# Optimization experiments

Measured on AMD Instinct MI355X. Metric: run time of the kernel, lower is better.

Reference implementation:

```python
import jax, jax.numpy as jnp
import numpy as np

B, OUT_LEN, IN_LEN, H = 8, 1024, 4096, 256


def setup_inputs() -> dict:
    key = jax.random.key(0)
    k1, k2, k3 = jax.random.split(key, 3)
    output = jax.random.normal(k1, (B, OUT_LEN, H), dtype=jnp.float32)
    encoder_outputs = jax.random.normal(k2, (B, IN_LEN, H), dtype=jnp.float32)
    # valid lengths in [1, IN_LEN] so every softmax row has >=1 unmasked entry
    lengths = jax.random.randint(k3, (B,), 1, IN_LEN + 1).astype(jnp.int32)
    return {"output": output, "encoder_outputs": encoder_outputs, "lengths": lengths}


def reference(output, encoder_outputs, lengths):
    # scores: [B, out_len, in_len], unscaled dot-product (as in the original)
    scores = jnp.einsum('boh,bih->boi', output, encoder_outputs)
    # mask[b, j] = j < lengths[b]; masked positions get -inf (additive mask)
    valid = jnp.arange(encoder_outputs.shape[1])[None, :] < lengths[:, None]  # [B, in_len]
    scores = jnp.where(valid[:, None, :], scores, -jnp.inf)
    attn = jax.nn.softmax(scores, axis=-1)  # [B, out_len, in_len]
    context = jnp.einsum('boi,bih->boh', attn, encoder_outputs)  # [B, out_len, H]
    return (context, attn)
```

## Files before the change

### kernel.cpp

```cpp
#include <hip/hip_runtime.h>
#include <hip/hip_bf16.h>
#include <math.h>

#define B_    8
#define OLEN  1024
#define ILEN  4096
#define HDIM  256
#define LDA   40

typedef __attribute__((ext_vector_type(8))) short bf16x8;
typedef __attribute__((ext_vector_type(4))) float f32x4;

__device__ inline unsigned pk_bf16(float x, float y) {
  union { __hip_bfloat162 h; unsigned u; } c;
  c.h = __float22bfloat162_rn(make_float2(x, y));
  return c.u;
}
__device__ inline short f2bf(float x) {
  union { __hip_bfloat16 h; short s; } c;
  c.h = __float2bfloat16(x);
  return c.s;
}

struct HiLo { uint4 hi, lo; };
__device__ inline HiLo split8(const float* __restrict__ p) {
  float4 v0 = *(const float4*)p;
  float4 v1 = *(const float4*)(p + 4);
  float f[8] = {v0.x, v0.y, v0.z, v0.w, v1.x, v1.y, v1.z, v1.w};
  unsigned hu[8]; float lo[8];
#pragma unroll
  for (int i = 0; i < 8; ++i) {
    unsigned u = __float_as_uint(f[i]);
    hu[i] = u & 0xffff0000u;
    lo[i] = f[i] - __uint_as_float(hu[i]);
  }
  HiLo r;
  r.hi = make_uint4((hu[0] >> 16) | hu[1], (hu[2] >> 16) | hu[3],
                    (hu[4] >> 16) | hu[5], (hu[6] >> 16) | hu[7]);
  r.lo = make_uint4(pk_bf16(lo[0], lo[1]), pk_bf16(lo[2], lo[3]),
                    pk_bf16(lo[4], lo[5]), pk_bf16(lo[6], lo[7]));
  return r;
}

__global__ __launch_bounds__(256) void k_etrans(const float* __restrict__ E,
                                                short* __restrict__ ET) {
  const int it = blockIdx.x, ht = blockIdx.y, b = blockIdx.z;
  __shared__ short L[32][36];
  const int t = threadIdx.x;
  {
    const int i = t >> 3, h0 = (t & 7) * 4;
    float4 v = *(const float4*)&E[((size_t)(b * ILEN + it * 32 + i)) * HDIM + ht * 32 + h0];
    L[h0 + 0][i] = f2bf(v.x);
    L[h0 + 1][i] = f2bf(v.y);
    L[h0 + 2][i] = f2bf(v.z);
    L[h0 + 3][i] = f2bf(v.w);
  }
  __syncthreads();
  {
    const int h = t >> 3, i0 = (t & 7) * 4;
    uint2 o = *(const uint2*)&L[h][i0];
    *(uint2*)&ET[((size_t)(b * HDIM + ht * 32 + h)) * ILEN + it * 32 + i0] = o;
  }
}

__global__ __launch_bounds__(256) void k_scores(const float* __restrict__ Q,
                                                const float* __restrict__ E,
                                                float* __restrict__ S) {
  const int b = blockIdx.z, ot = blockIdx.y, it = blockIdx.x;
  const float* Qb = Q + ((size_t)b * OLEN + ot * 64) * HDIM;
  const float* Eb = E + ((size_t)b * ILEN + it * 64) * HDIM;

  __shared__ __align__(16) short Ah[64 * LDA], Al[64 * LDA];
  __shared__ __align__(16) short Bh[64 * LDA], Bl[64 * LDA];

  const int t = threadIdx.x;
  const int w = t >> 6, l = t & 63;
  const int la = l & 15, quad = l >> 4;
  const int sr = t >> 2, sc = (t & 3) * 8;

  f32x4 acc[4] = {};

#pragma unroll
  for (int kc = 0; kc < HDIM; kc += 32) {
    HiLo qa = split8(&Qb[(size_t)sr * HDIM + kc + sc]);
    HiLo eb = split8(&Eb[(size_t)sr * HDIM + kc + sc]);
    *(uint4*)&Ah[sr * LDA + sc] = qa.hi;
    *(uint4*)&Al[sr * LDA + sc] = qa.lo;
    *(uint4*)&Bh[sr * LDA + sc] = eb.hi;
    *(uint4*)&Bl[sr * LDA + sc] = eb.lo;
    __syncthreads();
    bf16x8 ah = *(const bf16x8*)&Ah[(w * 16 + la) * LDA + quad * 8];
    bf16x8 al = *(const bf16x8*)&Al[(w * 16 + la) * LDA + quad * 8];
#pragma unroll
    for (int n = 0; n < 4; ++n) {
      bf16x8 bh = *(const bf16x8*)&Bh[(n * 16 + la) * LDA + quad * 8];
      bf16x8 bl = *(const bf16x8*)&Bl[(n * 16 + la) * LDA + quad * 8];
      acc[n] = __builtin_amdgcn_mfma_f32_16x16x32_bf16(ah, bh, acc[n], 0, 0, 0);
      acc[n] = __builtin_amdgcn_mfma_f32_16x16x32_bf16(ah, bl, acc[n], 0, 0, 0);
      acc[n] = __builtin_amdgcn_mfma_f32_16x16x32_bf16(al, bh, acc[n], 0, 0, 0);
    }
    __syncthreads();
  }

  float* Sb = S + ((size_t)b * OLEN + ot * 64) * (size_t)ILEN + it * 64;
#pragma unroll
  for (int n = 0; n < 4; ++n)
#pragma unroll
    for (int r = 0; r < 4; ++r)
      Sb[(size_t)(w * 16 + quad * 4 + r) * ILEN + n * 16 + la] = acc[n][r];
}

__global__ __launch_bounds__(256) void k_softmax(float* __restrict__ A,
                                                 const int* __restrict__ len) {
  const int row = blockIdx.x;
  const int b   = row >> 10;
  const int L   = len[b];
  float* p = A + (size_t)row * ILEN;
  const int t = threadIdx.x;

  float v[16];
#pragma unroll
  for (int k = 0; k < 4; ++k) {
    float4 x = *(const float4*)&p[4 * t + 1024 * k];
    v[4 * k + 0] = x.x; v[4 * k + 1] = x.y;
    v[4 * k + 2] = x.z; v[4 * k + 3] = x.w;
  }

  float m = -INFINITY;
#pragma unroll
  for (int k = 0; k < 4; ++k)
#pragma unroll
    for (int j = 0; j < 4; ++j) {
      const int i = 4 * t + 1024 * k + j;
      if (i < L) m = fmaxf(m, v[4 * k + j]);
    }
  for (int o = 32; o > 0; o >>= 1) m = fmaxf(m, __shfl_xor(m, o, 64));
  __shared__ float sm[4], ss[4];
  const int w = t >> 6;
  if ((t & 63) == 0) sm[w] = m;
  __syncthreads();
  m = fmaxf(fmaxf(sm[0], sm[1]), fmaxf(sm[2], sm[3]));

  float s = 0.f;
#pragma unroll
  for (int k = 0; k < 4; ++k)
#pragma unroll
    for (int j = 0; j < 4; ++j) {
      const int i = 4 * t + 1024 * k + j;
      float pv = (i < L) ? __expf(v[4 * k + j] - m) : 0.f;
      v[4 * k + j] = pv;
      s += pv;
    }
  for (int o = 32; o > 0; o >>= 1) s += __shfl_xor(s, o, 64);
  if ((t & 63) == 0) ss[w] = s;
  __syncthreads();
  s = ss[0] + ss[1] + ss[2] + ss[3];
  const float inv = 1.f / s;

#pragma unroll
  for (int k = 0; k < 4; ++k) {
    float4 x = make_float4(v[4 * k + 0] * inv, v[4 * k + 1] * inv,
                           v[4 * k + 2] * inv, v[4 * k + 3] * inv);
    *(float4*)&p[4 * t + 1024 * k] = x;
  }
}

__global__ __launch_bounds__(256) void k_context(const float* __restrict__ P,
                                                 const short* __restrict__ ET,
                                                 float* __restrict__ C) {
  const int ot = blockIdx.x, ht = blockIdx.y, b = blockIdx.z;
  const float* Pb = P + ((size_t)b * OLEN + ot * 64) * (size_t)ILEN;
  const short* Tb = ET + ((size_t)b * HDIM + ht * 64) * (size_t)ILEN;

  __shared__ __align__(16) short As[64 * LDA], Bs[64 * LDA];

  const int t = threadIdx.x;
  const int w = t >> 6, l = t & 63;
  const int la = l & 15, quad = l >> 4;
  const int sr = t >> 2, sc = (t & 3) * 8;

  f32x4 acc[4] = {};

  for (int ic = 0; ic < ILEN; ic += 32) {
    {
      float4 p0 = *(const float4*)&Pb[(size_t)sr * ILEN + ic + sc];
      float4 p1 = *(const float4*)&Pb[(size_t)sr * ILEN + ic + sc + 4];
      uint4 aw = make_uint4(pk_bf16(p0.x, p0.y), pk_bf16(p0.z, p0.w),
                            pk_bf16(p1.x, p1.y), pk_bf16(p1.z, p1.w));
      *(uint4*)&As[sr * LDA + sc] = aw;
      uint4 bw = *(const uint4*)&Tb[(size_t)sr * ILEN + ic + sc];
      *(uint4*)&Bs[sr * LDA + sc] = bw;
    }
    __syncthreads();
    bf16x8 a = *(const bf16x8*)&As[(w * 16 + la) * LDA + quad * 8];
#pragma unroll
    for (int n = 0; n < 4; ++n) {
      bf16x8 bb = *(const bf16x8*)&Bs[(n * 16 + la) * LDA + quad * 8];
      acc[n] = __builtin_amdgcn_mfma_f32_16x16x32_bf16(a, bb, acc[n], 0, 0, 0);
    }
    __syncthreads();
  }

  float* Cb = C + ((size_t)b * OLEN + ot * 64) * HDIM + ht * 64;
#pragma unroll
  for (int n = 0; n < 4; ++n)
#pragma unroll
    for (int r = 0; r < 4; ++r)
      Cb[(size_t)(w * 16 + quad * 4 + r) * HDIM + n * 16 + la] = acc[n][r];
}

extern "C" void kernel_launch(void* const* d_in, const int* in_sizes, int n_in,
                              void* d_out, int out_size, void* d_ws, size_t ws_size,
                              hipStream_t stream) {
  (void)in_sizes; (void)n_in; (void)out_size; (void)ws_size;
  const float* outp = (const float*)d_in[0];
  const float* enc  = (const float*)d_in[1];
  const int*   len  = (const int*)d_in[2];

  float* ctx  = (float*)d_out;
  float* attn = ctx + (size_t)B_ * OLEN * HDIM;
  short* ET   = (short*)d_ws;

  dim3 gt(ILEN / 32, HDIM / 32, B_);
  k_etrans<<<gt, 256, 0, stream>>>(enc, ET);
  dim3 g1(ILEN / 64, OLEN / 64, B_);
  k_scores<<<g1, 256, 0, stream>>>(outp, enc, attn);
  k_softmax<<<B_ * OLEN, 256, 0, stream>>>(attn, len);
  dim3 g3(OLEN / 64, HDIM / 64, B_);
  k_context<<<g3, 256, 0, stream>>>(attn, ET, ctx);
}
```

Measured before the change: 339.5 us.

## Pre-split Q/E into bf16 hi/lo and use 128x128 scores tiles with direct LDS loads

Adds prep kernels that split Q and E into bf16 hi/lo planes in workspace once. A new scores kernel then uses 128x128 output tiles with a 4x4 MFMA sub-tile per wave, filling LDS through global_load_lds with an XOR swizzle. This removes the repeated per-tile fp32-to-bf16 splitting and raises operand reuse per LDS fill. The cost is extra workspace and extra global write/read traffic, and the path only runs when the workspace holds at least 56 MiB. The fallback path passes ET as the hi/lo outputs to the prep kernel, so ET is overwritten with interleaved split data and the context kernel gets wrong results.

```diff
diff --git a/kernel.cpp b/kernel.cpp
--- a/kernel.cpp
+++ b/kernel.cpp
@@ -42,30 +42,131 @@
   return r;
 }
 
-__global__ __launch_bounds__(256) void k_etrans(const float* __restrict__ E,
+__device__ inline void gl_lds16(const void* g, void* l) {
+  __builtin_amdgcn_global_load_lds(
+      (const __attribute__((address_space(1))) unsigned*)g,
+      (__attribute__((address_space(3))) unsigned*)(l), 16, 0, 0);
+}
+
+__global__ __launch_bounds__(256) void k_prep_q(const float* __restrict__ Q,
+                                                short* __restrict__ Qhi,
+                                                short* __restrict__ Qlo) {
+  const size_t idx = ((size_t)blockIdx.x * 256 + threadIdx.x) * 8;
+  HiLo r = split8(&Q[idx]);
+  *(uint4*)&Qhi[idx] = r.hi;
+  *(uint4*)&Qlo[idx] = r.lo;
+}
+
+__global__ __launch_bounds__(256) void k_prep_e(const float* __restrict__ E,
+                                                short* __restrict__ Ehi,
+                                                short* __restrict__ Elo,
                                                 short* __restrict__ ET) {
   const int it = blockIdx.x, ht = blockIdx.y, b = blockIdx.z;
   __shared__ short L[32][36];
   const int t = threadIdx.x;
   {
     const int i = t >> 3, h0 = (t & 7) * 4;
-    float4 v = *(const float4*)&E[((size_t)(b * ILEN + it * 32 + i)) * HDIM + ht * 32 + h0];
-    L[h0 + 0][i] = f2bf(v.x);
-    L[h0 + 1][i] = f2bf(v.y);
-    L[h0 + 2][i] = f2bf(v.z);
-    L[h0 + 3][i] = f2bf(v.w);
+    const size_t gidx = ((size_t)(b * ILEN + it * 32 + i)) * HDIM + ht * 32 + h0;
+    float4 v = *(const float4*)&E[gidx];
+    float f[4] = {v.x, v.y, v.z, v.w};
+    unsigned hs[4]; float lo[4];
+#pragma unroll
+    for (int j = 0; j < 4; ++j) {
+      unsigned u = __float_as_uint(f[j]);
+      hs[j] = u & 0xffff0000u;
+      lo[j] = f[j] - __uint_as_float(hs[j]);
+    }
+    *(uint2*)&Ehi[gidx] = make_uint2((hs[0] >> 16) | hs[1], (hs[2] >> 16) | hs[3]);
+    *(uint2*)&Elo[gidx] = make_uint2(pk_bf16(lo[0], lo[1]), pk_bf16(lo[2], lo[3]));
+    L[h0 + 0][i] = f2bf(f[0]);
+    L[h0 + 1][i] = f2bf(f[1]);
+    L[h0 + 2][i] = f2bf(f[2]);
+    L[h0 + 3][i] = f2bf(f[3]);
   }
   __syncthreads();
   {
     const int h = t >> 3, i0 = (t & 7) * 4;
-    uint2 o = *(const uint2*)&L[h][i0];
-    *(uint2*)&ET[((size_t)(b * HDIM + ht * 32 + h)) * ILEN + it * 32 + i0] = o;
-  }
-}
-
-__global__ __launch_bounds__(256) void k_scores(const float* __restrict__ Q,
-                                                const float* __restrict__ E,
-                                                float* __restrict__ S) {
+    *(uint2*)&ET[((size_t)(b * HDIM + ht * 32 + h)) * ILEN + it * 32 + i0] =
+        *(const uint2*)&L[h][i0];
+  }
+}
+
+__global__ __launch_bounds__(256) void k_scores_pre(
+    const short* __restrict__ Qhi, const short* __restrict__ Qlo,
+    const short* __restrict__ Ehi, const short* __restrict__ Elo,
+    float* __restrict__ S) {
+  const int it = blockIdx.x, ot = blockIdx.y, b = blockIdx.z;
+  const size_t qoff = ((size_t)b * OLEN + ot * 128) * HDIM;
+  const size_t eoff = ((size_t)b * ILEN + it * 128) * HDIM;
+
+  __shared__ __align__(16) short Ah[128 * 32], Al[128 * 32];
+  __shared__ __align__(16) short Bh[128 * 32], Bl[128 * 32];
+
+  const int t = threadIdx.x;
+  const int w = t >> 6, l = t & 63;
+  const int la = l & 15, quad = l >> 4;
+  const int mw = (w & 1) * 64, nw = (w >> 1) * 64;
+
+  int sgoff[2], sloff[2];
+#pragma unroll
+  for (int j = 0; j < 2; ++j) {
+    const int row = (w * 2 + j) * 16 + (l >> 2);
+    const int c = (l & 3) ^ ((row >> 1) & 3);
+    sgoff[j] = row * HDIM + c * 8;
+    sloff[j] = ((w * 2 + j) * 64 + l) * 8;
+  }
+
+  f32x4 acc[4][4] = {};
+
+  for (int kc = 0; kc < HDIM; kc += 32) {
+#pragma unroll
+    for (int j = 0; j < 2; ++j) {
+      const size_t ga = qoff + sgoff[j] + kc;
+      const size_t gb = eoff + sgoff[j] + kc;
+      gl_lds16(&Qhi[ga], &Ah[sloff[j]]);
+      gl_lds16(&Qlo[ga], &Al[sloff[j]]);
+      gl_lds16(&Ehi[gb], &Bh[sloff[j]]);
+      gl_lds16(&Elo[gb], &Bl[sloff[j]]);
+    }
+    __syncthreads();
+    bf16x8 ah[4], al[4];
+#pragma unroll
+    for (int mi = 0; mi < 4; ++mi) {
+      const int row = mw + mi * 16 + la;
+      const int off = row * 32 + (quad ^ ((row >> 1) & 3)) * 8;
+      ah[mi] = *(const bf16x8*)&Ah[off];
+      al[mi] = *(const bf16x8*)&Al[off];
+    }
+#pragma unroll
+    for (int ni = 0; ni < 4; ++ni) {
+      const int row = nw + ni * 16 + la;
+      const int off = row * 32 + (quad ^ ((row >> 1) & 3)) * 8;
+      bf16x8 bh = *(const bf16x8*)&Bh[off];
+      bf16x8 bl = *(const bf16x8*)&Bl[off];
+#pragma unroll
+      for (int mi = 0; mi < 4; ++mi) {
+        acc[mi][ni] = __builtin_amdgcn_mfma_f32_16x16x32_bf16(ah[mi], bh, acc[mi][ni], 0, 0, 0);
+        acc[mi][ni] = __builtin_amdgcn_mfma_f32_16x16x32_bf16(ah[mi], bl, acc[mi][ni], 0, 0, 0);
+        acc[mi][ni] = __builtin_amdgcn_mfma_f32_16x16x32_bf16(al[mi], bh, acc[mi][ni], 0, 0, 0);
+      }
+    }
+    __syncthreads();
+  }
+
+  float* Sb = S + ((size_t)b * OLEN + ot * 128) * (size_t)ILEN + it * 128;
+#pragma unroll
+  for (int mi = 0; mi < 4; ++mi)
+#pragma unroll
+    for (int ni = 0; ni < 4; ++ni)
+#pragma unroll
+      for (int r = 0; r < 4; ++r)
+        Sb[(size_t)(mw + mi * 16 + quad * 4 + r) * ILEN + nw + ni * 16 + la] =
+            acc[mi][ni][r];
+}
+
+__global__ __launch_bounds__(256) void k_scores_split(const float* __restrict__ Q,
+                                                      const float* __restrict__ E,
+                                                      float* __restrict__ S) {
   const int b = blockIdx.z, ot = blockIdx.y, it = blockIdx.x;
   const float* Qb = Q + ((size_t)b * OLEN + ot * 64) * HDIM;
   const float* Eb = E + ((size_t)b * ILEN + it * 64) * HDIM;
@@ -212,19 +313,33 @@
 extern "C" void kernel_launch(void* const* d_in, const int* in_sizes, int n_in,
                               void* d_out, int out_size, void* d_ws, size_t ws_size,
                               hipStream_t stream) {
-  (void)in_sizes; (void)n_in; (void)out_size; (void)ws_size;
+  (void)in_sizes; (void)n_in; (void)out_size;
   const float* outp = (const float*)d_in[0];
   const float* enc  = (const float*)d_in[1];
   const int*   len  = (const int*)d_in[2];
 
   float* ctx  = (float*)d_out;
   float* attn = ctx + (size_t)B_ * OLEN * HDIM;
-  short* ET   = (short*)d_ws;
-
-  dim3 gt(ILEN / 32, HDIM / 32, B_);
-  k_etrans<<<gt, 256, 0, stream>>>(enc, ET);
-  dim3 g1(ILEN / 64, OLEN / 64, B_);
-  k_scores<<<g1, 256, 0, stream>>>(outp, enc, attn);
+
+  short* ws = (short*)d_ws;
+  const size_t M = 1024 * 1024;
+  short* ET = ws;
+
+  if (ws_size >= 56ull * 1024 * 1024) {
+    short* Qhi = ws + 8 * M;
+    short* Qlo = ws + 10 * M;
+    short* Ehi = ws + 12 * M;
+    short* Elo = ws + 20 * M;
+    k_prep_q<<<(B_ * OLEN * HDIM) / (256 * 8), 256, 0, stream>>>(outp, Qhi, Qlo);
+    dim3 gp(ILEN / 32, HDIM / 32, B_);
+    k_prep_e<<<gp, 256, 0, stream>>>(enc, Ehi, Elo, ET);
+    dim3 g1(ILEN / 128, OLEN / 128, B_);
+    k_scores_pre<<<g1, 256, 0, stream>>>(Qhi, Qlo, Ehi, Elo, attn);
+  } else {
+    dim3 gp(ILEN / 32, HDIM / 32, B_);
+    k_prep_e<<<gp, 256, 0, stream>>>(enc, ET, ET, ET);
+    k_scores_split<<<dim3(ILEN / 64, OLEN / 64, B_), 256, 0, stream>>>(outp, enc, attn);
+  }
   k_softmax<<<B_ * OLEN, 256, 0, stream>>>(attn, len);
   dim3 g3(OLEN / 64, HDIM / 64, B_);
   k_context<<<g3, 256, 0, stream>>>(attn, ET, ctx);
```

New measurement: 333.3 us. Within noise of the previous version (-1.8%).
